# Performance work log

Measured on AMD Instinct MI355X. Metric: run time of the kernel, lower is better.

The kernel has to match this reference:

```python
import jax, jax.numpy as jnp
import numpy as np

K = 3           # spatial kernel size (kernel_size[1]==kernel_size[2])
STRIDE = 1
EPS_BN = 1e-5


def unfold_replicate(t, k=K, stride=STRIDE):
    """t: (b, C, H, W) -> (b, C, k*k, H//stride, W//stride).
    Replicate-padded kxk patches, row-major window order (matches F.pad(replicate)+F.unfold)."""
    b, C, H, W = t.shape
    pad = (k - 1) // 2
    tp = jnp.pad(t, ((0, 0), (0, 0), (pad, pad), (pad, pad)), mode='edge')
    patches = [tp[:, :, di:di + H:stride, dj:dj + W:stride]
               for di in range(k) for dj in range(k)]
    return jnp.stack(patches, axis=2)


def grid_sample_3d(x, grid):
    """Trilinear grid sample, zeros padding, align_corners=True.
    x: (b,c,D,H,W); grid: (b,P,3) normalized (gx,gy,gz) -> (b,c,P)."""
    b, c, D, H, W = x.shape
    ix = (grid[..., 0] + 1.0) * 0.5 * (W - 1)
    iy = (grid[..., 1] + 1.0) * 0.5 * (H - 1)
    iz = (grid[..., 2] + 1.0) * 0.5 * (D - 1)
    x0 = jnp.floor(ix); y0 = jnp.floor(iy); z0 = jnp.floor(iz)
    fx = ix - x0; fy = iy - y0; fz = iz - z0
    x0i = x0.astype(jnp.int32); y0i = y0.astype(jnp.int32); z0i = z0.astype(jnp.int32)
    x_flat = x.reshape(b, c, D * H * W)
    gather = jax.vmap(lambda xf, idx: xf[:, idx])  # (c,N),(P) -> (c,P) per batch
    out = jnp.zeros((b, c, ix.shape[1]), dtype=x.dtype)
    for dz, wz in ((0, 1.0 - fz), (1, fz)):
        zi = z0i + dz
        for dy, wy in ((0, 1.0 - fy), (1, fy)):
            yi = y0i + dy
            for dx, wx in ((0, 1.0 - fx), (1, fx)):
                xi = x0i + dx
                valid = ((zi >= 0) & (zi < D) & (yi >= 0) & (yi < H)
                         & (xi >= 0) & (xi < W))
                idx = (jnp.clip(zi, 0, D - 1) * H + jnp.clip(yi, 0, H - 1)) * W \
                      + jnp.clip(xi, 0, W - 1)
                w = (wz * wy * wx) * valid.astype(x.dtype)
                out = out + w[:, None, :] * gather(x_flat, idx)
    return out


def gca_cost(x, dp, normal, intri):
    b, c, d, H, W = x.shape
    k2 = K * K
    h, w = H // STRIDE, W // STRIDE
    ctr = k2 // 2

    dp_unf = unfold_replicate(dp)        # (b, d, k2, h, w)
    n_unf = unfold_replicate(normal)     # (b, 3, k2, h, w)
    nx, ny, nz = n_unf[:, 0], n_unf[:, 1], n_unf[:, 2]

    fx = intri[:, 0, 0][:, None, None]; fy = intri[:, 1, 1][:, None, None]
    cx = intri[:, 0, 2][:, None, None]; cy = intri[:, 1, 2][:, None, None]
    yg, xg = jnp.meshgrid(jnp.arange(H, dtype=x.dtype),
                          jnp.arange(W, dtype=x.dtype), indexing='ij')
    posx = (xg[None] - cx) / fx          # (b, H, W) normalized camera rays
    posy = (yg[None] - cy) / fy
    pos_unf = unfold_replicate(jnp.stack([posx, posy], axis=1))  # (b,2,k2,h,w)
    pu, pv = pos_unf[:, 0], pos_unf[:, 1]
    pu_c = pu[:, ctr:ctr + 1]; pv_c = pv[:, ctr:ctr + 1]

    num = nx * pu_c + ny * pv_c + nz
    den = nx * pu + ny * pv + nz
    den = jnp.where(jnp.abs(den) < 1e-8, jnp.sign(den) * 1e-8, den)
    wgt = num / den
    wgt = jnp.where(jnp.isfinite(wgt), wgt, 1.0)   # (b, k2, h, w)

    dp_ctr = dp_unf[:, :, ctr]                      # (b, d, h, w)
    dp_prog = wgt[:, None] * dp_ctr[:, :, None]     # (b, d, k2, h, w)
    interval = dp_unf[:, 1] - dp_unf[:, 0]          # (b, k2, h, w)
    z = (dp_prog - dp_unf[:, 0][:, None]) / interval[:, None]  # (b,d,k2,h,w)

    xy = jnp.broadcast_to(jnp.stack([xg, yg], axis=0)[None], (b, 2, H, W))
    xy_unf = unfold_replicate(xy)                   # (b,2,k2,h,w)
    px = jnp.broadcast_to(xy_unf[:, 0][:, None], (b, d, k2, h, w))
    py = jnp.broadcast_to(xy_unf[:, 1][:, None], (b, d, k2, h, w))

    gx = px / ((W - 1) / 2.0) - 1.0
    gy = py / ((H - 1) / 2.0) - 1.0
    gz = z / ((d - 1) / 2.0) - 1.0
    grid = jnp.stack([gx, gy, gz], axis=-1).reshape(b, d * k2 * h * w, 3)

    samp = grid_sample_3d(x, grid)                  # (b, c, d*k2*h*w)
    samp = samp.reshape(b, c, d, k2, h, w).transpose(0, 1, 3, 2, 4, 5)
    return samp.reshape(b, c * k2, d, h, w)


def reference(x, dp, normal, intri, weight, gamma, beta):
    cost = gca_cost(x, dp, normal, intri)
    y = jax.lax.conv_general_dilated(
        cost, weight, window_strides=(1, 1, 1),
        padding=[(1, 1), (0, 0), (0, 0)],
        dimension_numbers=('NCDHW', 'OIDHW', 'NCDHW'))
    # BatchNorm3d (training-mode batch stats, biased var, eps=1e-5) + ReLU
    mean = jnp.mean(y, axis=(0, 2, 3, 4), keepdims=True)
    var = jnp.var(y, axis=(0, 2, 3, 4), keepdims=True)
    g = gamma.reshape(1, -1, 1, 1, 1)
    bta = beta.reshape(1, -1, 1, 1, 1)
    return jax.nn.relu(g * (y - mean) * jax.lax.rsqrt(var + EPS_BN) + bta)


def setup_inputs() -> dict:
    key = jax.random.key(0)
    ks = jax.random.split(key, 6)
    b, c, d, H, W = 1, 8, 32, 128, 128
    out_ch = 16
    x = jax.random.normal(ks[0], (b, c, d, H, W), dtype=jnp.float32)
    # monotone depth hypotheses per pixel (interval = dp[:,1]-dp[:,0] must be nonzero)
    planes = 425.0 + 10.0 * jnp.arange(d, dtype=jnp.float32)
    scale = 1.0 + 0.05 * jax.random.uniform(ks[1], (b, 1, H, W), dtype=jnp.float32)
    dp = planes[None, :, None, None] * scale                    # (b, d, H, W)
    # near-frontal unit normals so plane-homography weights stay well-conditioned
    nxy = 0.2 * jax.random.normal(ks[2], (b, 2, H, W), dtype=jnp.float32)
    nz = 1.0 + 0.1 * jax.random.normal(ks[3], (b, 1, H, W), dtype=jnp.float32)
    n = jnp.concatenate([nxy, nz], axis=1)
    normal = n / jnp.linalg.norm(n, axis=1, keepdims=True)
    intri = jnp.broadcast_to(
        jnp.array([[1100.0, 0.0, W / 2.0],
                   [0.0, 1100.0, H / 2.0],
                   [0.0, 0.0, 1.0]], dtype=jnp.float32), (b, 3, 3))
    weight = 0.05 * jax.random.normal(ks[4], (out_ch, c * K * K, 3, 1, 1),
                                      dtype=jnp.float32)
    gamma = jnp.ones((out_ch,), jnp.float32)
    beta = jnp.zeros((out_ch,), jnp.float32)
    return {"x": x, "dp": dp, "normal": normal, "intri": intri,
            "weight": weight, "gamma": gamma, "beta": beta}
```

## Files before the change

### kernel.cpp

```cpp
#include <hip/hip_runtime.h>
#include <math.h>

#define W_    128
#define H_    128
#define HW    16384
#define D_    32
#define C_IN  8
#define K2    9
#define OC    16
#define NRED  524288.0f

#define SXS   36
#define SXB   1948
#define TILE  2568

typedef __attribute__((ext_vector_type(8))) short bf16x8;
typedef __attribute__((ext_vector_type(4))) float f32x4;

union FragU { uint4 u; bf16x8 h; };


__device__ __forceinline__ unsigned bf16rne(float f) {
    unsigned u = __float_as_uint(f);
    return (u + 0x7fffu + ((u >> 16) & 1u)) >> 16;
}

__global__ __launch_bounds__(256) void k_init(const float* __restrict__ wsrc,
                                              float* __restrict__ ws) {
    int t = threadIdx.x;
    if (t < 32) ws[t] = 0.f;
    uint4* af = reinterpret_cast<uint4*>(ws + 64);
    for (int e = t; e < 768; e += 256) {
        int lane = e & 63, pkd = e >> 6;
        int p = pkd / 3, kd = pkd - p * 3;
        int o = lane & 15, kg = lane >> 4;
        int ch = 2 * p + (kg >> 1);
        int jb = (kg & 1) * 8;
        unsigned dw[4];
#pragma unroll
        for (int r2 = 0; r2 < 4; ++r2) {
            int j0 = jb + 2 * r2, j1 = j0 + 1;
            unsigned b0 = (j0 < 9) ? bf16rne(wsrc[(o * 72 + ch * 9 + j0) * 3 + kd]) : 0u;
            unsigned b1 = (j1 < 9) ? bf16rne(wsrc[(o * 72 + ch * 9 + j1) * 3 + kd]) : 0u;
            dw[r2] = b0 | (b1 << 16);
        }
        af[e] = make_uint4(dw[0], dw[1], dw[2], dw[3]);
    }
}

__global__ __launch_bounds__(256) void k_transpose(const float* __restrict__ x,
                                                   float* __restrict__ xt) {
    __shared__ float tile[32 * 132];
    int bid = blockIdx.x;
    int c  = bid >> 7;
    int ry = bid & 127;
    int t  = threadIdx.x;
    const float* src = x + c * (D_ * HW) + ry * W_;
    for (int k = 0; k < 4; ++k) {
        int e  = t * 4 + k * 1024;
        int z  = e >> 7;
        int rx = e & 127;
        float4 v = *reinterpret_cast<const float4*>(src + z * HW + rx);
        *reinterpret_cast<float4*>(&tile[z * 132 + rx]) = v;
    }
    __syncthreads();
    int rx = t >> 1;
    int zh = (t & 1) * 16;
    float* dst = xt + ((size_t)(c * HW + ry * W_ + rx)) * D_ + zh;
    for (int i = 0; i < 4; ++i) {
        float4 v;
        v.x = tile[(zh + i * 4 + 0) * 132 + rx];
        v.y = tile[(zh + i * 4 + 1) * 132 + rx];
        v.z = tile[(zh + i * 4 + 2) * 132 + rx];
        v.w = tile[(zh + i * 4 + 3) * 132 + rx];
        *reinterpret_cast<float4*>(dst + i * 4) = v;
    }
}

template <bool XT>
__global__ __launch_bounds__(512, 4) void k_main(const float* __restrict__ x,
                                                 const float* __restrict__ xt,
                                                 const float* __restrict__ dp,
                                                 const float* __restrict__ nrm,
                                                 const float* __restrict__ intri,
                                                 const uint4* __restrict__ afr,
                                                 float* __restrict__ out,
                                                 float* __restrict__ stats) {
    __shared__ float s_pool[2 * SXB];
    __shared__ float s_B[2 * TILE];
    __shared__ float s_wgt[144], s_dp0[144], s_inv[144];
    __shared__ float s_red[64];

    int t   = threadIdx.x;
    int bid = blockIdx.x;
    int r_row = bid >> 3;
    int rx0   = (bid & 7) * 16;

    int seg = t / 144;
    int f   = t - seg * 144;
    int spx = f >> 3;
    int zq  = f & 7;
    int srow = min(max(r_row + seg - 1, 0), H_ - 1);
    int scol = min(max(rx0 - 1 + spx, 0), W_ - 1);
    const float* gsrc     = xt + ((size_t)(srow * W_ + scol)) * D_ + zq * 4;
    const float* gsrc_raw = x + (srow * W_ + scol) + (size_t)(zq * 4) * HW;
    int sdst = 4 + (seg * 18 + spx) * SXS + zq * 4;

    float4 sv;
    if (t < 432) {
        if (XT) {
            sv = *reinterpret_cast<const float4*>(gsrc);
        } else {
            sv.x = gsrc_raw[0]; sv.y = gsrc_raw[HW];
            sv.z = gsrc_raw[2 * HW]; sv.w = gsrc_raw[3 * HW];
        }
    }

    if (t < 144) {
        int p = t / 9, j = t - p * 9;
        int jd = j / 3;
        int dy = jd - 1, dx = (j - jd * 3) - 1;
        int cpix = rx0 + p;
        int ry  = min(max(r_row + dy, 0), H_ - 1);
        int rxn = min(max(cpix + dx, 0), W_ - 1);
        int nb  = ry * W_ + rxn;
        float fx = intri[0], cx = intri[2], fy = intri[4], cy = intri[5];
        float nx = nrm[nb], ny = nrm[HW + nb], nz = nrm[2 * HW + nb];
        float pu  = ((float)rxn  - cx) / fx;
        float pv  = ((float)ry   - cy) / fy;
        float puc = ((float)cpix - cx) / fx;
        float pvc = ((float)r_row - cy) / fy;
        float num = nx * puc + ny * pvc + nz;
        float den = nx * pu + ny * pv + nz;
        if (fabsf(den) < 1e-8f)
            den = (den > 0.f) ? 1e-8f : ((den < 0.f) ? -1e-8f : 0.f);
        float w = num / den;
        if (!isfinite(w)) w = 1.0f;
        float d0  = dp[nb];
        float itv = dp[HW + nb] - d0;
        s_wgt[t] = w;
        s_dp0[t] = d0;
        s_inv[t] = 1.0f / itv;
    }
    if (t < 440) {
        int b  = t / 220;
        int rm = t - b * 220;
        int off = (rm < 4) ? rm : (4 + ((rm - 4) >> 2) * SXS + 32 + ((rm - 4) & 3));
        s_pool[b * SXB + off] = 0.f;
    }
    if (t < 16) s_B[2560 + (t >> 3) * TILE + (t & 7)] = 0.f;
    __syncthreads();
    if (t < 432) *reinterpret_cast<float4*>(&s_pool[sdst]) = sv;

    int px = t & 15;
    int d  = t >> 4;
    float dpv = dp[d * HW + r_row * W_ + rx0 + px];

    int   idx[9];
    float fza[9];
#pragma unroll
    for (int j = 0; j < 9; ++j) {
        int pj = px * 9 + j;
        int jd = j / 3;
        int jx = j - jd * 3;
        float z   = (s_wgt[pj] * dpv - s_dp0[pj]) * s_inv[pj];
        float zc  = fminf(fmaxf(z, -2.0f), 34.0f);
        float z0f = floorf(zc);
        fza[j] = zc - z0f;
        idx[j] = (jd * 18 + px + jx) * SXS + (int)z0f;
    }
    __syncthreads();

    f32x4 acc0 = {0.f, 0.f, 0.f, 0.f};
    f32x4 acc1 = {0.f, 0.f, 0.f, 0.f};
    f32x4 acc2 = {0.f, 0.f, 0.f, 0.f};
    f32x4 acc3 = {0.f, 0.f, 0.f, 0.f};

    int lane = t & 63;
    int wid  = t >> 6;
    int wb   = wid * 4;
    int grp  = lane >> 4;
    unsigned* sBu = reinterpret_cast<unsigned*>(s_B);
    int wrow = (d * 16 + px) * 5;

    for (int c = 0; c < C_IN; ++c) {
        if (c < 7 && t < 432) {
            if (XT) {
                sv = *reinterpret_cast<const float4*>(gsrc + (size_t)(c + 1) * (HW * D_));
            } else {
                const float* b = gsrc_raw + (size_t)(c + 1) * (D_ * HW);
                sv.x = b[0]; sv.y = b[HW]; sv.z = b[2 * HW]; sv.w = b[3 * HW];
            }
        }
        const float* sxp = &s_pool[(c & 1) * SXB + 4];
        float cj[9];
#pragma unroll
        for (int j = 0; j < 9; ++j) {
            float a = sxp[idx[j]];
            float b = sxp[idx[j] + 1];
            cj[j] = fmaf(fza[j], b - a, a);
        }
        unsigned dwv[5];
#pragma unroll
        for (int r2 = 0; r2 < 4; ++r2) {
            asm("v_cvt_pk_bf16_f32 %0, %1, %2"
                : "=v"(dwv[r2]) : "v"(cj[2 * r2]), "v"(cj[2 * r2 + 1]));
        }
        {
            float zz = 0.f;
            asm("v_cvt_pk_bf16_f32 %0, %1, %2"
                : "=v"(dwv[4]) : "v"(cj[8]), "v"(zz));
        }
        {
            int wo = wrow + (c & 1) * TILE;
            sBu[wo + 0] = dwv[0];
            sBu[wo + 1] = dwv[1];
            sBu[wo + 2] = dwv[2];
            sBu[wo + 3] = dwv[3];
            sBu[wo + 4] = dwv[4];
        }
        if (c < 7 && t < 432) *reinterpret_cast<float4*>(&s_pool[((c + 1) & 1) * SXB + sdst]) = sv;
        __syncthreads();

        if (c & 1) {
            int p = c >> 1;
            FragU a0, a1, a2;
            a0.u = afr[(p * 3 + 0) * 64 + lane];
            a1.u = afr[(p * 3 + 1) * 64 + lane];
            a2.u = afr[(p * 3 + 2) * 64 + lane];
            int boff = ((grp & 1) ? 4 : 0) + ((grp >> 1) ? TILE : 0);
#pragma unroll
            for (int q = 0; q < 6; ++q) {
                int db = wb - 1 + q;
                if (db < 0 || db > 31) continue;
                FragU bf;
                int base = (db * 16 + px) * 5 + boff;
                bf.u.x = sBu[base + 0];
                bf.u.y = sBu[base + 1];
                bf.u.z = sBu[base + 2];
                bf.u.w = sBu[base + 3];
                if (q - 0 >= 0 && q - 0 < 4)
                    *(q == 0 ? &acc0 : q == 1 ? &acc1 : q == 2 ? &acc2 : &acc3) =
                        __builtin_amdgcn_mfma_f32_16x16x32_bf16(a0.h, bf.h,
                            *(q == 0 ? &acc0 : q == 1 ? &acc1 : q == 2 ? &acc2 : &acc3), 0, 0, 0);
                if (q - 1 >= 0 && q - 1 < 4)
                    *(q == 1 ? &acc0 : q == 2 ? &acc1 : q == 3 ? &acc2 : &acc3) =
                        __builtin_amdgcn_mfma_f32_16x16x32_bf16(a1.h, bf.h,
                            *(q == 1 ? &acc0 : q == 2 ? &acc1 : q == 3 ? &acc2 : &acc3), 0, 0, 0);
                if (q - 2 >= 0 && q - 2 < 4)
                    *(q == 2 ? &acc0 : q == 3 ? &acc1 : q == 4 ? &acc2 : &acc3) =
                        __builtin_amdgcn_mfma_f32_16x16x32_bf16(a2.h, bf.h,
                            *(q == 2 ? &acc0 : q == 3 ? &acc1 : q == 4 ? &acc2 : &acc3), 0, 0, 0);
            }
            __syncthreads();
        }
    }

    float* s_b = s_pool;
    float bns[4], bnq[4];
    int o_l = t >> 7;
    int dd  = (t >> 2) & 31;
    int q4  = t & 3;
#pragma unroll
    for (int oo = 0; oo < 4; ++oo) {
        if (grp == oo) {
#pragma unroll
            for (int r2 = 0; r2 < 4; ++r2) {
                s_b[(r2 * 32 + wb + 0) * 17 + px] = acc0[r2];
                s_b[(r2 * 32 + wb + 1) * 17 + px] = acc1[r2];
                s_b[(r2 * 32 + wb + 2) * 17 + px] = acc2[r2];
                s_b[(r2 * 32 + wb + 3) * 17 + px] = acc3[r2];
            }
        }
        __syncthreads();
        const float* brow = &s_b[(o_l * 32 + dd) * 17 + q4 * 4];
        float4 yv;
        yv.x = brow[0]; yv.y = brow[1]; yv.z = brow[2]; yv.w = brow[3];
        int o = oo * 4 + o_l;
        *reinterpret_cast<float4*>(out + (size_t)(o * 32 + dd) * HW + r_row * W_ + rx0 + q4 * 4) = yv;
        bns[oo] = yv.x + yv.y + yv.z + yv.w;
        bnq[oo] = yv.x * yv.x + yv.y * yv.y + yv.z * yv.z + yv.w * yv.w;
        __syncthreads();
    }

#pragma unroll
    for (int oo = 0; oo < 4; ++oo) {
        float s = bns[oo], sq = bnq[oo];
#pragma unroll
        for (int m = 1; m < 64; m <<= 1) {
            s  += __shfl_xor(s, m, 64);
            sq += __shfl_xor(sq, m, 64);
        }
        if ((t & 63) == 0) {
            int w = t >> 6;
            s_red[w * 4 + oo]      = s;
            s_red[32 + w * 4 + oo] = sq;
        }
    }
    __syncthreads();
    if (t < 32) {
        int o  = t & 15;
        int oo = o >> 2, wh = o & 3;
        if (t < 16) {
            float s = s_red[(2 * wh) * 4 + oo] + s_red[(2 * wh + 1) * 4 + oo];
            atomicAdd(&stats[o], s);
        } else {
            float sq = s_red[32 + (2 * wh) * 4 + oo] + s_red[32 + (2 * wh + 1) * 4 + oo];
            atomicAdd(&stats[16 + o], sq);
        }
    }
}

__global__ __launch_bounds__(256) void k_bn(float* __restrict__ out,
                                            const float* __restrict__ stats,
                                            const float* __restrict__ gamma,
                                            const float* __restrict__ beta) {
    int i4 = blockIdx.x * 256 + threadIdx.x;
    int o  = i4 >> 17;
    float invN = 1.f / NRED;
    float mean = stats[o] * invN;
    float var  = stats[16 + o] * invN - mean * mean;
    float rstd = rsqrtf(var + 1e-5f);
    float a = gamma[o] * rstd;
    float b = beta[o] - mean * a;
    float4 y = reinterpret_cast<float4*>(out)[i4];
    y.x = fmaxf(0.f, fmaf(y.x, a, b));
    y.y = fmaxf(0.f, fmaf(y.y, a, b));
    y.z = fmaxf(0.f, fmaf(y.z, a, b));
    y.w = fmaxf(0.f, fmaf(y.w, a, b));
    reinterpret_cast<float4*>(out)[i4] = y;
}

extern "C" void kernel_launch(void* const* d_in, const int* in_sizes, int n_in,
                              void* d_out, int out_size, void* d_ws, size_t ws_size,
                              hipStream_t stream) {
    const float* x     = (const float*)d_in[0];
    const float* dp    = (const float*)d_in[1];
    const float* nrm   = (const float*)d_in[2];
    const float* intri = (const float*)d_in[3];
    const float* wsrc  = (const float*)d_in[4];
    const float* gamma = (const float*)d_in[5];
    const float* beta  = (const float*)d_in[6];
    float* out = (float*)d_out;
    float* ws  = (float*)d_ws;

    bool xt_ok = ws_size >= (size_t)(8192 + 4194304) * 4;
    float* xt = ws + 8192;
    const uint4* afr = (const uint4*)(ws + 64);

    hipLaunchKernelGGL(k_init, dim3(1), dim3(256), 0, stream, wsrc, ws);
    if (xt_ok) {
        hipLaunchKernelGGL(k_transpose, dim3(1024), dim3(256), 0, stream, x, xt);
        hipLaunchKernelGGL(k_main<true>, dim3(1024), dim3(512), 0, stream,
                           x, xt, dp, nrm, intri, afr, out, ws);
    } else {
        hipLaunchKernelGGL(k_main<false>, dim3(1024), dim3(512), 0, stream,
                           x, xt, dp, nrm, intri, afr, out, ws);
    }
    hipLaunchKernelGGL(k_bn, dim3(8192), dim3(256), 0, stream, out, ws, gamma, beta);
}
```

Measured before the change: 67.25 us.

## Fuse batchnorm+ReLU into main conv kernel via cooperative grid sync

The main kernel now handles two 16-pixel tiles per block and keeps the accumulators in registers. Batch-norm statistics are computed from those accumulators before anything is stored, then a cooperative grid-wide sync lets each block apply BN and ReLU while writing output. This removes the separate k_bn pass, which reread and rewrote the whole output tensor. The cost is a grid barrier, higher register pressure from holding two tiles of accumulators, and a fallback path with the old two-kernel sequence when a cooperative launch is not possible.

```diff
diff --git a/kernel.cpp b/kernel.cpp
--- a/kernel.cpp
+++ b/kernel.cpp
@@ -1,12 +1,14 @@
 #include <hip/hip_runtime.h>
+#include <hip/hip_cooperative_groups.h>
 #include <math.h>
+
+namespace cg = cooperative_groups;
 
 #define W_    128
 #define H_    128
 #define HW    16384
 #define D_    32
 #define C_IN  8
-#define K2    9
 #define OC    16
 #define NRED  524288.0f
 
@@ -78,24 +80,15 @@
 }
 
 template <bool XT>
-__global__ __launch_bounds__(512, 4) void k_main(const float* __restrict__ x,
-                                                 const float* __restrict__ xt,
-                                                 const float* __restrict__ dp,
-                                                 const float* __restrict__ nrm,
-                                                 const float* __restrict__ intri,
-                                                 const uint4* __restrict__ afr,
-                                                 float* __restrict__ out,
-                                                 float* __restrict__ stats) {
-    __shared__ float s_pool[2 * SXB];
-    __shared__ float s_B[2 * TILE];
-    __shared__ float s_wgt[144], s_dp0[144], s_inv[144];
-    __shared__ float s_red[64];
-
-    int t   = threadIdx.x;
-    int bid = blockIdx.x;
-    int r_row = bid >> 3;
-    int rx0   = (bid & 7) * 16;
-
+__device__ __forceinline__ void conv_tile(
+    const float* __restrict__ x, const float* __restrict__ xt,
+    const float* __restrict__ dp, const float* __restrict__ nrm,
+    const float* __restrict__ intri, const uint4* __restrict__ afr,
+    float* __restrict__ stats, int t, int r_row, int rx0,
+    float* s_pool, float* s_B, float* s_wgt, float* s_dp0, float* s_inv,
+    float* s_red,
+    f32x4& acc0, f32x4& acc1, f32x4& acc2, f32x4& acc3)
+{
     int seg = t / 144;
     int f   = t - seg * 144;
     int spx = f >> 3;
@@ -171,10 +164,10 @@
     }
     __syncthreads();
 
-    f32x4 acc0 = {0.f, 0.f, 0.f, 0.f};
-    f32x4 acc1 = {0.f, 0.f, 0.f, 0.f};
-    f32x4 acc2 = {0.f, 0.f, 0.f, 0.f};
-    f32x4 acc3 = {0.f, 0.f, 0.f, 0.f};
+    acc0 = f32x4{0.f, 0.f, 0.f, 0.f};
+    acc1 = f32x4{0.f, 0.f, 0.f, 0.f};
+    acc2 = f32x4{0.f, 0.f, 0.f, 0.f};
+    acc3 = f32x4{0.f, 0.f, 0.f, 0.f};
 
     int lane = t & 63;
     int wid  = t >> 6;
@@ -256,11 +249,53 @@
         }
     }
 
-    float* s_b = s_pool;
-    float bns[4], bnq[4];
-    int o_l = t >> 7;
-    int dd  = (t >> 2) & 31;
-    int q4  = t & 3;
+    {
+        float sA[4], qA[4];
+#pragma unroll
+        for (int r2 = 0; r2 < 4; ++r2) {
+            sA[r2] = acc0[r2] + acc1[r2] + acc2[r2] + acc3[r2];
+            qA[r2] = acc0[r2] * acc0[r2] + acc1[r2] * acc1[r2]
+                   + acc2[r2] * acc2[r2] + acc3[r2] * acc3[r2];
+#pragma unroll
+            for (int m = 1; m < 16; m <<= 1) {
+                sA[r2] += __shfl_xor(sA[r2], m, 16);
+                qA[r2] += __shfl_xor(qA[r2], m, 16);
+            }
+        }
+        if ((lane & 15) == 0) {
+            int base = wid * 16 + grp * 4;
+#pragma unroll
+            for (int r2 = 0; r2 < 4; ++r2) {
+                s_red[base + r2]       = sA[r2];
+                s_red[128 + base + r2] = qA[r2];
+            }
+        }
+    }
+    __syncthreads();
+    if (t < 32) {
+        int o = t & 15;
+        float s = 0.f;
+        if (t < 16) {
+            for (int w = 0; w < 8; ++w) s += s_red[w * 16 + o];
+            atomicAdd(&stats[o], s);
+        } else {
+            for (int w = 0; w < 8; ++w) s += s_red[128 + w * 16 + o];
+            atomicAdd(&stats[16 + o], s);
+        }
+    }
+    __syncthreads();
+}
+
+template <bool FUSED>
+__device__ __forceinline__ void store_tile(
+    float* __restrict__ out, const float* __restrict__ gamma,
+    const float* __restrict__ beta,
+    float* s_b, const float* s_stats, int t, int r_row, int rx0,
+    const f32x4& acc0, const f32x4& acc1, const f32x4& acc2, const f32x4& acc3)
+{
+    int px   = t & 15;
+    int lane = t & 63, wid = t >> 6, wb = wid * 4, grp = lane >> 4;
+    int o_l = t >> 7, dd = (t >> 2) & 31, q4 = t & 3;
 #pragma unroll
     for (int oo = 0; oo < 4; ++oo) {
         if (grp == oo) {
@@ -273,42 +308,60 @@
             }
         }
         __syncthreads();
+        int o = oo * 4 + o_l;
         const float* brow = &s_b[(o_l * 32 + dd) * 17 + q4 * 4];
         float4 yv;
         yv.x = brow[0]; yv.y = brow[1]; yv.z = brow[2]; yv.w = brow[3];
-        int o = oo * 4 + o_l;
+        if (FUSED) {
+            float invN = 1.f / NRED;
+            float mean = s_stats[o] * invN;
+            float var  = s_stats[16 + o] * invN - mean * mean;
+            float rstd = rsqrtf(var + 1e-5f);
+            float aS = gamma[o] * rstd;
+            float bS = beta[o] - mean * aS;
+            yv.x = fmaxf(0.f, fmaf(yv.x, aS, bS));
+            yv.y = fmaxf(0.f, fmaf(yv.y, aS, bS));
+            yv.z = fmaxf(0.f, fmaf(yv.z, aS, bS));
+            yv.w = fmaxf(0.f, fmaf(yv.w, aS, bS));
+        }
         *reinterpret_cast<float4*>(out + (size_t)(o * 32 + dd) * HW + r_row * W_ + rx0 + q4 * 4) = yv;
-        bns[oo] = yv.x + yv.y + yv.z + yv.w;
-        bnq[oo] = yv.x * yv.x + yv.y * yv.y + yv.z * yv.z + yv.w * yv.w;
         __syncthreads();
     }
-
-#pragma unroll
-    for (int oo = 0; oo < 4; ++oo) {
-        float s = bns[oo], sq = bnq[oo];
-#pragma unroll
-        for (int m = 1; m < 64; m <<= 1) {
-            s  += __shfl_xor(s, m, 64);
-            sq += __shfl_xor(sq, m, 64);
-        }
-        if ((t & 63) == 0) {
-            int w = t >> 6;
-            s_red[w * 4 + oo]      = s;
-            s_red[32 + w * 4 + oo] = sq;
-        }
-    }
-    __syncthreads();
-    if (t < 32) {
-        int o  = t & 15;
-        int oo = o >> 2, wh = o & 3;
-        if (t < 16) {
-            float s = s_red[(2 * wh) * 4 + oo] + s_red[(2 * wh + 1) * 4 + oo];
-            atomicAdd(&stats[o], s);
-        } else {
-            float sq = s_red[32 + (2 * wh) * 4 + oo] + s_red[32 + (2 * wh + 1) * 4 + oo];
-            atomicAdd(&stats[16 + o], sq);
-        }
-    }
+}
+
+template <bool XT, bool FUSED>
+__global__ __launch_bounds__(512, 6) void k_main(
+    const float* __restrict__ x, const float* __restrict__ xt,
+    const float* __restrict__ dp, const float* __restrict__ nrm,
+    const float* __restrict__ intri, const uint4* __restrict__ afr,
+    float* __restrict__ out, float* __restrict__ stats,
+    const float* __restrict__ gamma, const float* __restrict__ beta)
+{
+    __shared__ float s_pool[2 * SXB];
+    __shared__ float s_B[2 * TILE];
+    __shared__ float s_wgt[144], s_dp0[144], s_inv[144];
+    __shared__ float s_red[256];
+
+    int t   = threadIdx.x;
+    int bid = blockIdx.x;
+    int r_row = bid >> 2;
+    int rxA   = ((bid & 3) << 1) * 16;
+    int rxB   = rxA + 16;
+
+    f32x4 aA0, aA1, aA2, aA3, aB0, aB1, aB2, aB3;
+    conv_tile<XT>(x, xt, dp, nrm, intri, afr, stats, t, r_row, rxA,
+                  s_pool, s_B, s_wgt, s_dp0, s_inv, s_red, aA0, aA1, aA2, aA3);
+    conv_tile<XT>(x, xt, dp, nrm, intri, afr, stats, t, r_row, rxB,
+                  s_pool, s_B, s_wgt, s_dp0, s_inv, s_red, aB0, aB1, aB2, aB3);
+
+    if (FUSED) {
+        __threadfence();
+        cg::this_grid().sync();
+        if (t < 32) s_red[t] = atomicAdd(&stats[t], 0.0f);
+        __syncthreads();
+    }
+    store_tile<FUSED>(out, gamma, beta, s_pool, s_red, t, r_row, rxA, aA0, aA1, aA2, aA3);
+    store_tile<FUSED>(out, gamma, beta, s_pool, s_red, t, r_row, rxB, aB0, aB1, aB2, aB3);
 }
 
 __global__ __launch_bounds__(256) void k_bn(float* __restrict__ out,
@@ -351,11 +404,25 @@
     hipLaunchKernelGGL(k_init, dim3(1), dim3(256), 0, stream, wsrc, ws);
     if (xt_ok) {
         hipLaunchKernelGGL(k_transpose, dim3(1024), dim3(256), 0, stream, x, xt);
-        hipLaunchKernelGGL(k_main<true>, dim3(1024), dim3(512), 0, stream,
-                           x, xt, dp, nrm, intri, afr, out, ws);
+        int maxb = 0;
+        hipError_t qe = hipOccupancyMaxActiveBlocksPerMultiprocessor(
+            &maxb, reinterpret_cast<const void*>(&k_main<true, true>), 512, 0);
+        hipError_t ce = hipErrorUnknown;
+        if (qe == hipSuccess && maxb >= 3) {
+            void* args[] = {(void*)&x, (void*)&xt, (void*)&dp, (void*)&nrm, (void*)&intri,
+                            (void*)&afr, (void*)&out, (void*)&ws, (void*)&gamma, (void*)&beta};
+            ce = hipLaunchCooperativeKernel(
+                reinterpret_cast<void*>(&k_main<true, true>),
+                dim3(512), dim3(512), args, 0, stream);
+        }
+        if (ce != hipSuccess) {
+            hipLaunchKernelGGL((k_main<true, false>), dim3(512), dim3(512), 0, stream,
+                               x, xt, dp, nrm, intri, afr, out, ws, gamma, beta);
+            hipLaunchKernelGGL(k_bn, dim3(8192), dim3(256), 0, stream, out, ws, gamma, beta);
+        }
     } else {
-        hipLaunchKernelGGL(k_main<false>, dim3(1024), dim3(512), 0, stream,
-                           x, xt, dp, nrm, intri, afr, out, ws);
-    }
-    hipLaunchKernelGGL(k_bn, dim3(8192), dim3(256), 0, stream, out, ws, gamma, beta);
-}
+        hipLaunchKernelGGL((k_main<false, false>), dim3(512), dim3(512), 0, stream,
+                           x, nullptr, dp, nrm, intri, afr, out, ws, gamma, beta);
+        hipLaunchKernelGGL(k_bn, dim3(8192), dim3(256), 0, stream, out, ws, gamma, beta);
+    }
+}
```

New measurement: 96.27 us. 43.1% more time.
